# Optimization experiments

Hardware: AMD Instinct MI355X
Metric: run time of the kernel (lower is better)

## Reference

```python
import jax, jax.numpy as jnp
import numpy as np

B, T, E, H = 4, 1024, 768, 12
HD = E // H                      # 64
R = 2                            # lora rank
LORA_SCALE = 1.0 / R             # loralib default lora_alpha=1 -> alpha/r
NUM_BUCKETS, MAX_DIST = 320, 800


def _rel_bucket(rel):
    nb = NUM_BUCKETS // 2                      # 160
    buckets = (rel > 0).astype(jnp.int32) * nb
    rel = jnp.abs(rel)
    max_exact = nb // 2                        # 80
    is_small = rel < max_exact
    log_ratio = jnp.log(jnp.maximum(rel, 1).astype(jnp.float32) / max_exact)
    large = max_exact + (log_ratio / np.log(MAX_DIST / max_exact) * (nb - max_exact)).astype(jnp.int32)
    large = jnp.minimum(large, nb - 1)
    return buckets + jnp.where(is_small, rel, large)


def setup_inputs() -> dict:
    key = jax.random.key(0)
    ks = jax.random.split(key, 22)
    s = 0.02
    w = lambda k, shape: jax.random.normal(k, shape, jnp.float32) * s
    return {
        "hidden_states": jax.random.normal(ks[0], (B, T, E), jnp.float32),
        "Wq": w(ks[1], (E, E)), "bq": w(ks[2], (E,)),
        "Wk": w(ks[3], (E, E)), "bk": w(ks[4], (E,)),
        "Wv": w(ks[5], (E, E)), "bv": w(ks[6], (E,)),
        "Aq": w(ks[7], (R, E)), "Bq": w(ks[8], (E, R)),
        "Ak": w(ks[9], (R, E)), "Bk": w(ks[10], (E, R)),
        "Av": w(ks[11], (R, E)), "Bv": w(ks[12], (E, R)),
        "Wo": w(ks[13], (E, E)), "bo": w(ks[14], (E,)),
        "Wg": w(ks[15], (8, HD)), "bg": w(ks[16], (8,)),
        "gru_const": jnp.ones((1, H, 1, 1), jnp.float32),
        "rel_embed": w(ks[17], (NUM_BUCKETS, H)),
    }


def reference(hidden_states, Wq, bq, Wk, bk, Wv, bv,
              Aq, Bq, Ak, Bk, Av, Bv, Wo, bo, Wg, bg, gru_const, rel_embed):
    Bsz, Tq, _ = hidden_states.shape
    # --- relative position bias [H, T, T] ---
    pos = jnp.arange(Tq)
    bucket = _rel_bucket(pos[None, :] - pos[:, None])
    pos_bias = rel_embed[bucket].transpose(2, 0, 1)
    # --- dynamic gate from hidden states, per head/position ---
    g = hidden_states.reshape(Bsz, Tq, H, HD).transpose(0, 2, 1, 3)      # [B,H,T,hd]
    gp = jnp.einsum('bhtd,ed->bhte', g, Wg) + bg                          # [B,H,T,8]
    gp = gp.reshape(Bsz, H, Tq, 2, 4).sum(-1)                             # [B,H,T,2]
    gates = jax.nn.sigmoid(gp)
    gate_a, gate_b = gates[..., :1], gates[..., 1:]
    gate = gate_a * (gate_b * gru_const - 1.0) + 2.0                      # [B,H,T,1]
    gated_bias = gate * pos_bias[None]                                    # [B,H,T,T]
    # --- projections: original double-applies q/k/v_proj (proj+LoRA, then
    #     again inside F.multi_head_attention_forward via separate proj weights) ---
    lin = lambda x, W, b: jnp.einsum('bte,oe->bto', x, W) + b
    lora = lambda x, A, Bm: jnp.einsum('bte,re,or->bto', x, A, Bm) * LORA_SCALE
    x = hidden_states
    q1 = lin(x, Wq, bq) + lora(x, Aq, Bq)
    k1 = lin(x, Wk, bk) + lora(x, Ak, Bk)
    v1 = lin(x, Wv, bv) + lora(x, Av, Bv)
    q = lin(q1, Wq, bq) * (HD ** -0.5)
    k = lin(k1, Wk, bk)
    v = lin(v1, Wv, bv)
    qh = q.reshape(Bsz, Tq, H, HD).transpose(0, 2, 1, 3)
    kh = k.reshape(Bsz, Tq, H, HD).transpose(0, 2, 1, 3)
    vh = v.reshape(Bsz, Tq, H, HD).transpose(0, 2, 1, 3)
    scores = jnp.einsum('bhqd,bhkd->bhqk', qh, kh) + gated_bias
    attn = jax.nn.softmax(scores, axis=-1)
    ctx = jnp.einsum('bhqk,bhkd->bhqd', attn, vh)
    out = ctx.transpose(0, 2, 1, 3).reshape(Bsz, Tq, E)
    return jnp.einsum('bte,oe->bto', out, Wo) + bo
```

## Files before the change

### kernel.cpp

```cpp
#include <hip/hip_runtime.h>
#include <math.h>

#define TT 1024
#define EE 768
#define HH 12

typedef __attribute__((ext_vector_type(8))) __bf16 bf16x8;
typedef __attribute__((ext_vector_type(4))) float f32x4;

__device__ __forceinline__ unsigned short f2b(float f) {
    unsigned int u = __float_as_uint(f);
    unsigned int r = (u + 0x7fffu + ((u >> 16) & 1u)) >> 16;
    return (unsigned short)r;
}

#define GLD16(gsrc, ldst) \
    __builtin_amdgcn_global_load_lds( \
        (const __attribute__((address_space(1))) unsigned int*)(gsrc), \
        (__attribute__((address_space(3))) unsigned int*)(ldst), 16, 0, 0)

__global__ __launch_bounds__(256)
void setup_k(const float* __restrict__ hs,
             const float* __restrict__ Wq, const float* __restrict__ Wk,
             const float* __restrict__ Wv, const float* __restrict__ Wo,
             const float* __restrict__ bq, const float* __restrict__ bk,
             const float* __restrict__ bv,
             const float* __restrict__ Aq, const float* __restrict__ Ak,
             const float* __restrict__ Av,
             const float* __restrict__ Bq, const float* __restrict__ Bk,
             const float* __restrict__ Bv,
             const float* __restrict__ Wg, const float* __restrict__ bg,
             const float* __restrict__ gru, const float* __restrict__ rel,
             unsigned short* __restrict__ Wall_b, unsigned short* __restrict__ WT_all,
             float* __restrict__ biasTab, float* __restrict__ bias2,
             float* __restrict__ B2,
             unsigned short* __restrict__ hsb, float* __restrict__ gate,
             float* __restrict__ xA) {
    __shared__ __align__(16) char smem[78080];
    const int bid = blockIdx.x, tid = threadIdx.x;

    if (bid < 1152) {
        size_t base = (size_t)bid * 2048 + tid * 8;
        int mat = (int)(base / 589824);
        size_t local = base % 589824;
        const float* S = mat == 0 ? Wq : (mat == 1 ? Wk : (mat == 2 ? Wv : Wo));
        float4 a = *(const float4*)&S[local];
        float4 c = *(const float4*)&S[local + 4];
        unsigned short hb[8] __attribute__((aligned(16)));
        hb[0] = f2b(a.x); hb[1] = f2b(a.y); hb[2] = f2b(a.z); hb[3] = f2b(a.w);
        hb[4] = f2b(c.x); hb[5] = f2b(c.y); hb[6] = f2b(c.z); hb[7] = f2b(c.w);
        *(uint4*)&Wall_b[base] = *(const uint4*)hb;
    } else if (bid < 1260) {
        unsigned short* Ts = (unsigned short*)smem;
        int v = bid - 1152;
        int mat = v / 36, tile = v % 36;
        int tr = tile / 6, tc = tile % 6;
        const float* S = mat == 0 ? Wq : (mat == 1 ? Wk : Wv);
        #pragma unroll
        for (int i = 0; i < 16; ++i) {
            int idx = i * 256 + tid;
            int row = idx >> 5, col4 = (idx & 31) * 4;
            float4 f = *(const float4*)&S[(size_t)(tr * 128 + row) * EE + tc * 128 + col4];
            Ts[(col4 + 0) * 136 + row] = f2b(f.x);
            Ts[(col4 + 1) * 136 + row] = f2b(f.y);
            Ts[(col4 + 2) * 136 + row] = f2b(f.z);
            Ts[(col4 + 3) * 136 + row] = f2b(f.w);
        }
        __syncthreads();
        unsigned short* dst = WT_all + (size_t)mat * 589824;
        #pragma unroll
        for (int i = 0; i < 8; ++i) {
            int idx = i * 256 + tid;
            int rr = idx >> 4, cg = (idx & 15) * 8;
            *(uint4*)&dst[(size_t)(tc * 128 + rr) * EE + tr * 128 + cg] =
                *(const uint4*)&Ts[rr * 136 + cg];
        }
    } else if (bid < 1356) {
        int idx = (bid - 1260) * 256 + tid;
        if (idx < 2047 * 12) {
            int h = idx % 12;
            int rr = idx / 12;
            int relv = rr - 1023;
            int base = relv > 0 ? 160 : 0;
            int ar = relv < 0 ? -relv : relv;
            int bkt;
            if (ar < 80) bkt = base + ar;
            else {
                double lr = log((double)ar / 80.0);
                int large = 80 + (int)(lr / log(10.0) * 80.0);
                if (large > 159) large = 159;
                bkt = base + large;
            }
            biasTab[h * 2048 + rr] = rel[bkt * 12 + h];
        }
    } else if (bid < 1368) {
        float* bvS = (float*)smem;
        float* BmS = bvS + 768;
        int v = bid - 1356;
        int sel = v / 4, nb = (v % 4) * 192;
        const float* W = sel == 0 ? Wq : (sel == 1 ? Wk : Wv);
        const float* bvec = sel == 0 ? bq : (sel == 1 ? bk : bv);
        const float* Bm = sel == 0 ? Bq : (sel == 1 ? Bk : Bv);
        for (int i = tid; i < 768; i += 256) bvS[i] = bvec[i];
        for (int i = tid; i < 1536; i += 256) BmS[i] = Bm[i];
        __syncthreads();
        if (tid < 192) {
            int n = nb + tid;
            const float* Wrow = W + (size_t)n * EE;
            float a0 = 0.f, a1 = 0.f, a2 = 0.f;
            for (int o = 0; o < EE; o += 4) {
                float4 w = *(const float4*)&Wrow[o];
                a0 += w.x * bvS[o] + w.y * bvS[o + 1] + w.z * bvS[o + 2] + w.w * bvS[o + 3];
                a1 += w.x * BmS[o * 2] + w.y * BmS[o * 2 + 2] + w.z * BmS[o * 2 + 4] + w.w * BmS[o * 2 + 6];
                a2 += w.x * BmS[o * 2 + 1] + w.y * BmS[o * 2 + 3] + w.z * BmS[o * 2 + 5] + w.w * BmS[o * 2 + 7];
            }
            float sc = (sel == 0) ? 0.125f : 1.0f;
            bias2[sel * 768 + n] = (a0 + bvS[n]) * sc;
            B2[sel * 1536 + n * 2 + 0] = a1 * sc;
            B2[sel * 1536 + n * 2 + 1] = a2 * sc;
        }
    } else {
        float* rowF = (float*)smem;
        float* AS   = rowF + 16 * 772;
        float* WgS  = AS + 6 * 768;
        float* gpS  = WgS + 8 * 68;
        float* redS = gpS + 16 * 100;
        float* bgS  = redS + 4 * 96;
        float* gcS  = bgS + 8;
        const int m0 = (bid - 1368) * 16;

        for (int i = tid; i < 512; i += 256) WgS[(i >> 6) * 68 + (i & 63)] = Wg[i];
        for (int i = tid; i < 1152; i += 256) {
            int which = i / 192, c4 = (i % 192) * 4;
            const float* src = (which < 2 ? Aq : (which < 4 ? Ak : Av)) + (which & 1) * 768 + c4;
            float4 f = *(const float4*)src;
            AS[which * 768 + c4 + 0] = f.x; AS[which * 768 + c4 + 1] = f.y;
            AS[which * 768 + c4 + 2] = f.z; AS[which * 768 + c4 + 3] = f.w;
        }
        if (tid < 8)  bgS[tid] = bg[tid];
        if (tid < 12) gcS[tid] = gru[tid];
        #pragma unroll
        for (int i = 0; i < 12; ++i) {
            int idx = i * 256 + tid;
            int row = idx / 192, c4 = (idx % 192) * 4;
            float4 f = *(const float4*)&hs[(size_t)(m0 + row) * EE + c4];
            rowF[row * 772 + c4 + 0] = f.x; rowF[row * 772 + c4 + 1] = f.y;
            rowF[row * 772 + c4 + 2] = f.z; rowF[row * 772 + c4 + 3] = f.w;
            unsigned int lo = (unsigned int)f2b(f.x) | ((unsigned int)f2b(f.y) << 16);
            unsigned int hi = (unsigned int)f2b(f.z) | ((unsigned int)f2b(f.w) << 16);
            uint2 p; p.x = lo; p.y = hi;
            *(uint2*)&hsb[(size_t)(m0 + row) * EE + c4] = p;
        }
        __syncthreads();
        #pragma unroll
        for (int j = 0; j < 6; ++j) {
            int idx = j * 256 + tid;
            int row = idx & 15, q = idx >> 4;
            int h = q % 12, e = q / 12;
            const float* rp = &rowF[row * 772 + h * 64];
            const float* wp = &WgS[e * 68];
            float a = 0.f;
            #pragma unroll 16
            for (int d = 0; d < 64; ++d) a += rp[d] * wp[d];
            gpS[row * 100 + h * 8 + e] = a;
        }
        {
            int row = tid & 15, seg = tid >> 4;
            float s[6] = {0.f, 0.f, 0.f, 0.f, 0.f, 0.f};
            #pragma unroll 8
            for (int j = 0; j < 48; ++j) {
                int e = seg * 48 + j;
                float xv = rowF[row * 772 + e];
                s[0] += xv * AS[e];            s[1] += xv * AS[768 + e];
                s[2] += xv * AS[1536 + e];     s[3] += xv * AS[2304 + e];
                s[4] += xv * AS[3072 + e];     s[5] += xv * AS[3840 + e];
            }
            #pragma unroll
            for (int i = 0; i < 6; ++i) {
                s[i] += __shfl_xor(s[i], 16, 64);
                s[i] += __shfl_xor(s[i], 32, 64);
            }
            int lane = tid & 63, w = tid >> 6;
            if ((lane >> 4) == 0)
                #pragma unroll
                for (int i = 0; i < 6; ++i) redS[w * 96 + row * 6 + i] = s[i];
        }
        __syncthreads();
        if (tid < 96) {
            int row = tid / 6, i = tid % 6;
            float v = redS[row * 6 + i] + redS[96 + row * 6 + i] +
                      redS[192 + row * 6 + i] + redS[288 + row * 6 + i];
            int sel = i >> 1, r = i & 1;
            xA[sel * 8192 + (size_t)(m0 + row) * 2 + r] = v;
        }
        if (tid < 192) {
            int row = tid / 12, h = tid % 12;
            const float* gp = &gpS[row * 100 + h * 8];
            float s0 = gp[0] + gp[1] + gp[2] + gp[3] + bgS[0] + bgS[1] + bgS[2] + bgS[3];
            float s1 = gp[4] + gp[5] + gp[6] + gp[7] + bgS[4] + bgS[5] + bgS[6] + bgS[7];
            float ga = 1.f / (1.f + __expf(-s0));
            float gb = 1.f / (1.f + __expf(-s1));
            int m = m0 + row;
            int b = m >> 10, tp = m & 1023;
            gate[((size_t)b * HH + h) * TT + tp] = ga * (gb * gcS[h] - 1.0f) + 2.0f;
        }
    }
}

__global__ __launch_bounds__(256, 3)
void wgemm_k(const unsigned short* __restrict__ Wall_b,
             const unsigned short* __restrict__ WT_all,
             unsigned short* __restrict__ W2_all) {
    __shared__ unsigned short At[128 * 32];
    __shared__ unsigned short Bt[128 * 32];
    const int tid = threadIdx.x;
    const int bxx = blockIdx.x;
    const int sel = bxx / 36, tile = bxx % 36;
    const int row0 = (tile / 6) * 128, col0 = (tile % 6) * 128;
    const unsigned short* A = Wall_b + (size_t)sel * 589824;
    const unsigned short* Bw = WT_all + (size_t)sel * 589824;

    const int lane = tid & 63, wv = tid >> 6;
    const int wm = (wv & 1) * 64, wn = (wv >> 1) * 64;
    const int l15 = lane & 15, g8 = (lane >> 4) * 8;
    const int lr = lane >> 2, lc = (lane & 3) * 8;
    const int c0 = wv * 2, c1 = wv * 2 + 1;
    const unsigned short* Abase0 = A + (size_t)(row0 + c0 * 16 + lr) * EE + lc;
    const unsigned short* Abase1 = A + (size_t)(row0 + c1 * 16 + lr) * EE + lc;
    const unsigned short* Bbase0 = Bw + (size_t)(col0 + c0 * 16 + lr) * EE + lc;
    const unsigned short* Bbase1 = Bw + (size_t)(col0 + c1 * 16 + lr) * EE + lc;

    f32x4 zero4 = {0.f, 0.f, 0.f, 0.f};
    f32x4 acc[4][4];
    #pragma unroll
    for (int i = 0; i < 4; ++i)
        #pragma unroll
        for (int j = 0; j < 4; ++j) acc[i][j] = zero4;

    for (int kt = 0; kt < 768; kt += 32) {
        GLD16(Abase0 + kt, &At[c0 * 512]);
        GLD16(Abase1 + kt, &At[c1 * 512]);
        GLD16(Bbase0 + kt, &Bt[c0 * 512]);
        GLD16(Bbase1 + kt, &Bt[c1 * 512]);
        __syncthreads();
        bf16x8 af[4], bf[4];
        #pragma unroll
        for (int mt = 0; mt < 4; ++mt) af[mt] = *(const bf16x8*)&At[(wm + mt * 16 + l15) * 32 + g8];
        #pragma unroll
        for (int nt = 0; nt < 4; ++nt) bf[nt] = *(const bf16x8*)&Bt[(wn + nt * 16 + l15) * 32 + g8];
        #pragma unroll
        for (int mt = 0; mt < 4; ++mt)
            #pragma unroll
            for (int nt = 0; nt < 4; ++nt)
                acc[mt][nt] = __builtin_amdgcn_mfma_f32_16x16x32_bf16(af[mt], bf[nt], acc[mt][nt], 0, 0, 0);
        __syncthreads();
    }
    unsigned short* out = W2_all + (size_t)sel * 589824;
    const float sc = (sel == 0) ? 0.125f : 1.0f;
    const int g4 = (lane >> 4) * 4;
    #pragma unroll
    for (int mt = 0; mt < 4; ++mt)
        #pragma unroll
        for (int r = 0; r < 4; ++r) {
            int grow = row0 + wm + mt * 16 + g4 + r;
            #pragma unroll
            for (int nt = 0; nt < 4; ++nt) {
                int ncol = col0 + wn + nt * 16 + l15;
                out[(size_t)grow * EE + ncol] = f2b(acc[mt][nt][r] * sc);
            }
        }
}

__global__ __launch_bounds__(256, 3)
void qkv_gemm_k(const unsigned short* __restrict__ Aall,
                const unsigned short* __restrict__ W2_all,
                const float* __restrict__ bias2,
                const float* __restrict__ xA, const float* __restrict__ B2,
                unsigned short* __restrict__ qb, unsigned short* __restrict__ kb,
                unsigned short* __restrict__ vb) {
    __shared__ unsigned short At[128 * 32];
    __shared__ unsigned short Bt[128 * 32];
    const int tid = threadIdx.x;
    const int bx = blockIdx.x, by = blockIdx.y;
    const int sel = bx / 6;
    const int col0 = (bx % 6) * 128, row0 = by * 128;
    const unsigned short* Wb = W2_all + (size_t)sel * 589824;
    const float* bias = bias2 + sel * 768;

    const int lane = tid & 63, wv = tid >> 6;
    const int wm = (wv & 1) * 64, wn = (wv >> 1) * 64;
    const int l15 = lane & 15, g8 = (lane >> 4) * 8;
    const int lr = lane >> 2, lc = (lane & 3) * 8;
    const int c0 = wv * 2, c1 = wv * 2 + 1;
    const unsigned short* Abase0 = Aall + (size_t)(row0 + c0 * 16 + lr) * EE + lc;
    const unsigned short* Abase1 = Aall + (size_t)(row0 + c1 * 16 + lr) * EE + lc;
    const unsigned short* Bbase0 = Wb + (size_t)(col0 + c0 * 16 + lr) * EE + lc;
    const unsigned short* Bbase1 = Wb + (size_t)(col0 + c1 * 16 + lr) * EE + lc;

    f32x4 zero4 = {0.f, 0.f, 0.f, 0.f};
    f32x4 acc[4][4];
    #pragma unroll
    for (int i = 0; i < 4; ++i)
        #pragma unroll
        for (int j = 0; j < 4; ++j) acc[i][j] = zero4;

    for (int kt = 0; kt < 768; kt += 32) {
        GLD16(Abase0 + kt, &At[c0 * 512]);
        GLD16(Abase1 + kt, &At[c1 * 512]);
        GLD16(Bbase0 + kt, &Bt[c0 * 512]);
        GLD16(Bbase1 + kt, &Bt[c1 * 512]);
        __syncthreads();
        bf16x8 af[4], bf[4];
        #pragma unroll
        for (int mt = 0; mt < 4; ++mt) af[mt] = *(const bf16x8*)&At[(wm + mt * 16 + l15) * 32 + g8];
        #pragma unroll
        for (int nt = 0; nt < 4; ++nt) bf[nt] = *(const bf16x8*)&Bt[(wn + nt * 16 + l15) * 32 + g8];
        #pragma unroll
        for (int mt = 0; mt < 4; ++mt)
            #pragma unroll
            for (int nt = 0; nt < 4; ++nt)
                acc[mt][nt] = __builtin_amdgcn_mfma_f32_16x16x32_bf16(af[mt], bf[nt], acc[mt][nt], 0, 0, 0);
        __syncthreads();
    }

    unsigned short* dst = sel == 0 ? qb : (sel == 1 ? kb : vb);
    const float* Lbase = xA + sel * 8192;
    const float* B2s   = B2 + sel * 1536;
    const int g4 = (lane >> 4) * 4;
    #pragma unroll
    for (int mt = 0; mt < 4; ++mt) {
        #pragma unroll
        for (int r = 0; r < 4; ++r) {
            size_t grow = (size_t)row0 + wm + mt * 16 + g4 + r;
            float l0 = Lbase[grow * 2], l1 = Lbase[grow * 2 + 1];
            #pragma unroll
            for (int nt = 0; nt < 4; ++nt) {
                int ncol = col0 + wn + nt * 16 + l15;
                float c = acc[mt][nt][r] + bias[ncol]
                          + 0.5f * (l0 * B2s[ncol * 2] + l1 * B2s[ncol * 2 + 1]);
                dst[grow * EE + ncol] = f2b(c);
            }
        }
    }
}

__global__ __launch_bounds__(256)
void vT_k(const unsigned short* __restrict__ vb, unsigned short* __restrict__ Vtg) {
    __shared__ unsigned short Vs[64 * 72];
    const int tid = threadIdx.x;
    const int tt = blockIdx.x, h = blockIdx.y, b = blockIdx.z;
    const int r = tid >> 3, cc = (tid & 7) * 8;
    #pragma unroll
    for (int i = 0; i < 2; ++i) {
        int row = i * 32 + r;
        const unsigned short* vp = vb + (size_t)(b * TT + tt * 64 + row) * EE + h * 64 + cc;
        *(uint4*)&Vs[row * 72 + cc] = *(const uint4*)vp;
    }
    __syncthreads();
    #pragma unroll
    for (int i = 0; i < 2; ++i) {
        int d = i * 32 + r;
        unsigned short tmp[8] __attribute__((aligned(16)));
        #pragma unroll
        for (int j = 0; j < 8; ++j) tmp[j] = Vs[(cc + j) * 72 + d];
        *(uint4*)&Vtg[((size_t)(b * HH + h) * 64 + d) * TT + tt * 64 + cc] = *(const uint4*)tmp;
    }
}

__global__ __launch_bounds__(256, 4)
void attn_k(const unsigned short* __restrict__ qb, const unsigned short* __restrict__ kb,
            const unsigned short* __restrict__ Vtg, const float* __restrict__ gate,
            const float* __restrict__ biasTab, unsigned short* __restrict__ ctx) {
    __shared__ unsigned short Qs[64 * 72];
    __shared__ unsigned short Ks[64 * 72];
    __shared__ unsigned short Vt[64 * 72];
    __shared__ unsigned short Ps[64 * 72];
    const int tid = threadIdx.x;
    const int qt = blockIdx.x, h = blockIdx.y, b = blockIdx.z;

    const int srow = tid >> 2, scol = (tid & 3) * 16;
    {
        const unsigned short* qp = qb + ((size_t)(b * TT + qt * 64 + srow)) * EE + h * 64 + scol;
        *(uint4*)&Qs[srow * 72 + scol]     = *(const uint4*)qp;
        *(uint4*)&Qs[srow * 72 + scol + 8] = *(const uint4*)(qp + 8);
    }
    const int lane = tid & 63, wv = tid >> 6;
    const int m0 = wv * 16;
    const int l15 = lane & 15, g = lane >> 4;

    float li[4];
    f32x4 zero4 = {0.f, 0.f, 0.f, 0.f};
    f32x4 oa[4];
    #pragma unroll
    for (int r = 0; r < 4; ++r) li[r] = 0.f;
    #pragma unroll
    for (int nt = 0; nt < 4; ++nt) oa[nt] = zero4;
    float gv[4];
    #pragma unroll
    for (int r = 0; r < 4; ++r)
        gv[r] = gate[((size_t)(b * HH + h)) * TT + qt * 64 + m0 + 4 * g + r];

    const unsigned short* kpbase = kb + ((size_t)(b * TT + srow)) * EE + h * 64 + scol;
    const unsigned short* vpbase = Vtg + ((size_t)(b * HH + h) * 64 + srow) * TT + scol;
    const float* btab = biasTab + h * 2048 + 1023 + l15 - qt * 64 - m0 - 4 * g;

    uint4 kr0 = *(const uint4*)kpbase;
    uint4 kr1 = *(const uint4*)(kpbase + 8);
    uint4 vr0 = *(const uint4*)vpbase;
    uint4 vr1 = *(const uint4*)(vpbase + 8);

    for (int kt = 0; kt < 16; ++kt) {
        __syncthreads();
        *(uint4*)&Ks[srow * 72 + scol]     = kr0;
        *(uint4*)&Ks[srow * 72 + scol + 8] = kr1;
        *(uint4*)&Vt[srow * 72 + scol]     = vr0;
        *(uint4*)&Vt[srow * 72 + scol + 8] = vr1;
        __syncthreads();
        if (kt < 15) {
            const unsigned short* kp = kpbase + (size_t)(kt + 1) * 64 * EE;
            kr0 = *(const uint4*)kp;
            kr1 = *(const uint4*)(kp + 8);
            const unsigned short* vp = vpbase + (kt + 1) * 64;
            vr0 = *(const uint4*)vp;
            vr1 = *(const uint4*)(vp + 8);
        }
        f32x4 sa[4];
        #pragma unroll
        for (int nt = 0; nt < 4; ++nt) sa[nt] = zero4;
        bf16x8 aq0 = *(const bf16x8*)&Qs[(m0 + l15) * 72 + g * 8];
        bf16x8 aq1 = *(const bf16x8*)&Qs[(m0 + l15) * 72 + 32 + g * 8];
        #pragma unroll
        for (int nt = 0; nt < 4; ++nt) {
            bf16x8 bk0 = *(const bf16x8*)&Ks[(nt * 16 + l15) * 72 + g * 8];
            bf16x8 bk1 = *(const bf16x8*)&Ks[(nt * 16 + l15) * 72 + 32 + g * 8];
            sa[nt] = __builtin_amdgcn_mfma_f32_16x16x32_bf16(aq0, bk0, sa[nt], 0, 0, 0);
            sa[nt] = __builtin_amdgcn_mfma_f32_16x16x32_bf16(aq1, bk1, sa[nt], 0, 0, 0);
        }
        #pragma unroll
        for (int nt = 0; nt < 4; ++nt) {
            const float* bt = btab + kt * 64 + nt * 16;
            #pragma unroll
            for (int r = 0; r < 4; ++r) {
                float e = __expf(fmaf(gv[r], bt[-r], sa[nt][r]));
                li[r] += e;
                Ps[(m0 + 4 * g + r) * 72 + nt * 16 + l15] = f2b(e);
            }
        }
        bf16x8 ap0 = *(const bf16x8*)&Ps[(m0 + l15) * 72 + g * 8];
        bf16x8 ap1 = *(const bf16x8*)&Ps[(m0 + l15) * 72 + 32 + g * 8];
        #pragma unroll
        for (int nt = 0; nt < 4; ++nt) {
            bf16x8 bv0 = *(const bf16x8*)&Vt[(nt * 16 + l15) * 72 + g * 8];
            bf16x8 bv1 = *(const bf16x8*)&Vt[(nt * 16 + l15) * 72 + 32 + g * 8];
            oa[nt] = __builtin_amdgcn_mfma_f32_16x16x32_bf16(ap0, bv0, oa[nt], 0, 0, 0);
            oa[nt] = __builtin_amdgcn_mfma_f32_16x16x32_bf16(ap1, bv1, oa[nt], 0, 0, 0);
        }
    }
    __syncthreads();
    #pragma unroll
    for (int r = 0; r < 4; ++r) {
        #pragma unroll
        for (int msk = 1; msk < 16; msk <<= 1)
            li[r] += __shfl_xor(li[r], msk, 16);
    }
    #pragma unroll
    for (int nt = 0; nt < 4; ++nt)
        #pragma unroll
        for (int r = 0; r < 4; ++r)
            Ks[(m0 + 4 * g + r) * 72 + nt * 16 + l15] = f2b(oa[nt][r] / li[r]);
    __syncthreads();
    {
        unsigned short* cp = ctx + ((size_t)(b * TT + qt * 64 + srow)) * EE + h * 64 + scol;
        *(uint4*)cp       = *(const uint4*)&Ks[srow * 72 + scol];
        *(uint4*)(cp + 8) = *(const uint4*)&Ks[srow * 72 + scol + 8];
    }
}

__global__ __launch_bounds__(256, 4)
void out_gemm_k(const unsigned short* __restrict__ Aall,
                const unsigned short* __restrict__ Wob,
                const float* __restrict__ bo, float* __restrict__ outf) {
    __shared__ unsigned short At[64 * 32];
    __shared__ unsigned short Bt[128 * 32];
    const int tid = threadIdx.x;
    const int col0 = blockIdx.x * 128, row0 = blockIdx.y * 64;

    const int lane = tid & 63, wv = tid >> 6;
    const int wm = (wv & 1) * 32, wn = (wv >> 1) * 64;
    const int l15 = lane & 15, g8 = (lane >> 4) * 8;
    const int lr = lane >> 2, lc = (lane & 3) * 8;
    const int c0 = wv * 2, c1 = wv * 2 + 1;
    const unsigned short* Abase  = Aall + (size_t)(row0 + wv * 16 + lr) * EE + lc;
    const unsigned short* Bbase0 = Wob + (size_t)(col0 + c0 * 16 + lr) * EE + lc;
    const unsigned short* Bbase1 = Wob + (size_t)(col0 + c1 * 16 + lr) * EE + lc;

    f32x4 zero4 = {0.f, 0.f, 0.f, 0.f};
    f32x4 acc[2][4];
    #pragma unroll
    for (int i = 0; i < 2; ++i)
        #pragma unroll
        for (int j = 0; j < 4; ++j) acc[i][j] = zero4;

    for (int kt = 0; kt < 768; kt += 32) {
        GLD16(Abase + kt, &At[wv * 512]);
        GLD16(Bbase0 + kt, &Bt[c0 * 512]);
        GLD16(Bbase1 + kt, &Bt[c1 * 512]);
        __syncthreads();
        bf16x8 af[2], bf[4];
        #pragma unroll
        for (int mt = 0; mt < 2; ++mt) af[mt] = *(const bf16x8*)&At[(wm + mt * 16 + l15) * 32 + g8];
        #pragma unroll
        for (int nt = 0; nt < 4; ++nt) bf[nt] = *(const bf16x8*)&Bt[(wn + nt * 16 + l15) * 32 + g8];
        #pragma unroll
        for (int mt = 0; mt < 2; ++mt)
            #pragma unroll
            for (int nt = 0; nt < 4; ++nt)
                acc[mt][nt] = __builtin_amdgcn_mfma_f32_16x16x32_bf16(af[mt], bf[nt], acc[mt][nt], 0, 0, 0);
        __syncthreads();
    }
    const int g4 = (lane >> 4) * 4;
    #pragma unroll
    for (int mt = 0; mt < 2; ++mt)
        #pragma unroll
        for (int r = 0; r < 4; ++r) {
            size_t grow = (size_t)row0 + wm + mt * 16 + g4 + r;
            #pragma unroll
            for (int nt = 0; nt < 4; ++nt) {
                int ncol = col0 + wn + nt * 16 + l15;
                outf[grow * EE + ncol] = acc[mt][nt][r] + bo[ncol];
            }
        }
}

extern "C" void kernel_launch(void* const* d_in, const int* in_sizes, int n_in,
                              void* d_out, int out_size, void* d_ws, size_t ws_size,
                              hipStream_t stream) {
    const float* hs  = (const float*)d_in[0];
    const float* Wq  = (const float*)d_in[1];
    const float* bq  = (const float*)d_in[2];
    const float* Wk  = (const float*)d_in[3];
    const float* bk  = (const float*)d_in[4];
    const float* Wv  = (const float*)d_in[5];
    const float* bv  = (const float*)d_in[6];
    const float* Aq  = (const float*)d_in[7];
    const float* Bq  = (const float*)d_in[8];
    const float* Ak  = (const float*)d_in[9];
    const float* Bk  = (const float*)d_in[10];
    const float* Av  = (const float*)d_in[11];
    const float* Bv  = (const float*)d_in[12];
    const float* Wo  = (const float*)d_in[13];
    const float* bo  = (const float*)d_in[14];
    const float* Wg  = (const float*)d_in[15];
    const float* bg  = (const float*)d_in[16];
    const float* gru = (const float*)d_in[17];
    const float* rel = (const float*)d_in[18];

    float* ws = (float*)d_ws;
    float* gate    = ws;
    float* biasTab = gate + 49152;
    float* xA      = biasTab + 24576;
    float* bias2   = xA + 24576;
    float* B2      = bias2 + 2304;
    unsigned short* hsb    = (unsigned short*)(B2 + 4608);
    unsigned short* Wall_b = hsb + 3145728;
    unsigned short* WT_all = Wall_b + 4 * 589824;
    unsigned short* W2_all = WT_all + 3 * 589824;
    unsigned short* qb     = W2_all + 3 * 589824;
    unsigned short* kb     = qb + 3145728;
    unsigned short* vb     = kb + 3145728;
    unsigned short* Vtg    = vb + 3145728;
    unsigned short* ctxb   = Vtg + 3145728;

    setup_k<<<1624, 256, 0, stream>>>(hs, Wq, Wk, Wv, Wo, bq, bk, bv,
                                      Aq, Ak, Av, Bq, Bk, Bv, Wg, bg, gru, rel,
                                      Wall_b, WT_all, biasTab, bias2, B2,
                                      hsb, gate, xA);
    wgemm_k<<<108, 256, 0, stream>>>(Wall_b, WT_all, W2_all);
    qkv_gemm_k<<<dim3(18, 32), 256, 0, stream>>>(hsb, W2_all, bias2, xA, B2, qb, kb, vb);
    vT_k<<<dim3(16, 12, 4), 256, 0, stream>>>(vb, Vtg);
    attn_k<<<dim3(16, 12, 4), 256, 0, stream>>>(qb, kb, Vtg, gate, biasTab, ctxb);
    out_gemm_k<<<dim3(6, 64), 256, 0, stream>>>(ctxb, Wall_b + 3 * 589824, bo, (float*)d_out);
}
```

Measured before the change: 230.7 us.

## Split setup kernel and halve GEMM row tiles to fill more CUs

The monolithic setup kernel is split into three kernels: a flat fp32-to-bf16 converter for hidden states and weights, a transpose/bias/bucket-table kernel, and a gate/LoRA-down kernel working on 8-row blocks with less shared memory. The weight-product and QKV GEMMs drop their M tile from 128 to 64 rows, which doubles block counts and raises the occupancy hint to 4. The goal is more parallelism and better CU utilisation on small grids. In exchange it adds two kernel launches, reads hidden states twice, and loses some operand reuse per GEMM tile.

```diff
diff --git a/kernel.cpp b/kernel.cpp
--- a/kernel.cpp
+++ b/kernel.cpp
@@ -20,40 +20,38 @@
         (__attribute__((address_space(3))) unsigned int*)(ldst), 16, 0, 0)
 
 __global__ __launch_bounds__(256)
-void setup_k(const float* __restrict__ hs,
-             const float* __restrict__ Wq, const float* __restrict__ Wk,
-             const float* __restrict__ Wv, const float* __restrict__ Wo,
-             const float* __restrict__ bq, const float* __restrict__ bk,
-             const float* __restrict__ bv,
-             const float* __restrict__ Aq, const float* __restrict__ Ak,
-             const float* __restrict__ Av,
-             const float* __restrict__ Bq, const float* __restrict__ Bk,
-             const float* __restrict__ Bv,
-             const float* __restrict__ Wg, const float* __restrict__ bg,
-             const float* __restrict__ gru, const float* __restrict__ rel,
-             unsigned short* __restrict__ Wall_b, unsigned short* __restrict__ WT_all,
-             float* __restrict__ biasTab, float* __restrict__ bias2,
-             float* __restrict__ B2,
-             unsigned short* __restrict__ hsb, float* __restrict__ gate,
-             float* __restrict__ xA) {
-    __shared__ __align__(16) char smem[78080];
+void conv_k(const float* __restrict__ hs, const float* __restrict__ Wq,
+            const float* __restrict__ Wk, const float* __restrict__ Wv,
+            const float* __restrict__ Wo, unsigned short* __restrict__ out) {
+    size_t i = 4 * (size_t)(blockIdx.x * 256 + threadIdx.x);
+    if (i >= 5505024) return;
+    const float* src;
+    if (i < 3145728)      src = hs + i;
+    else if (i < 3735552) src = Wq + (i - 3145728);
+    else if (i < 4325376) src = Wk + (i - 3735552);
+    else if (i < 4915200) src = Wv + (i - 4325376);
+    else                  src = Wo + (i - 4915200);
+    float4 f = *(const float4*)src;
+    unsigned int lo = (unsigned int)f2b(f.x) | ((unsigned int)f2b(f.y) << 16);
+    unsigned int hi = (unsigned int)f2b(f.z) | ((unsigned int)f2b(f.w) << 16);
+    uint2 p; p.x = lo; p.y = hi;
+    *(uint2*)&out[i] = p;
+}
+
+__global__ __launch_bounds__(256)
+void wT2_k(const float* __restrict__ Wq, const float* __restrict__ Wk,
+           const float* __restrict__ Wv,
+           const float* __restrict__ bq, const float* __restrict__ bk,
+           const float* __restrict__ bv,
+           const float* __restrict__ Bq, const float* __restrict__ Bk,
+           const float* __restrict__ Bv, const float* __restrict__ rel,
+           unsigned short* __restrict__ WT_all, float* __restrict__ biasTab,
+           float* __restrict__ bias2, float* __restrict__ B2) {
+    __shared__ __align__(16) char smem[34816];
     const int bid = blockIdx.x, tid = threadIdx.x;
-
-    if (bid < 1152) {
-        size_t base = (size_t)bid * 2048 + tid * 8;
-        int mat = (int)(base / 589824);
-        size_t local = base % 589824;
-        const float* S = mat == 0 ? Wq : (mat == 1 ? Wk : (mat == 2 ? Wv : Wo));
-        float4 a = *(const float4*)&S[local];
-        float4 c = *(const float4*)&S[local + 4];
-        unsigned short hb[8] __attribute__((aligned(16)));
-        hb[0] = f2b(a.x); hb[1] = f2b(a.y); hb[2] = f2b(a.z); hb[3] = f2b(a.w);
-        hb[4] = f2b(c.x); hb[5] = f2b(c.y); hb[6] = f2b(c.z); hb[7] = f2b(c.w);
-        *(uint4*)&Wall_b[base] = *(const uint4*)hb;
-    } else if (bid < 1260) {
+    if (bid < 108) {
         unsigned short* Ts = (unsigned short*)smem;
-        int v = bid - 1152;
-        int mat = v / 36, tile = v % 36;
+        int mat = bid / 36, tile = bid % 36;
         int tr = tile / 6, tc = tile % 6;
         const float* S = mat == 0 ? Wq : (mat == 1 ? Wk : Wv);
         #pragma unroll
@@ -75,8 +73,8 @@
             *(uint4*)&dst[(size_t)(tc * 128 + rr) * EE + tr * 128 + cg] =
                 *(const uint4*)&Ts[rr * 136 + cg];
         }
-    } else if (bid < 1356) {
-        int idx = (bid - 1260) * 256 + tid;
+    } else if (bid < 204) {
+        int idx = (bid - 108) * 256 + tid;
         if (idx < 2047 * 12) {
             int h = idx % 12;
             int rr = idx / 12;
@@ -93,10 +91,10 @@
             }
             biasTab[h * 2048 + rr] = rel[bkt * 12 + h];
         }
-    } else if (bid < 1368) {
+    } else {
         float* bvS = (float*)smem;
         float* BmS = bvS + 768;
-        int v = bid - 1356;
+        int v = bid - 204;
         int sel = v / 4, nb = (v % 4) * 192;
         const float* W = sel == 0 ? Wq : (sel == 1 ? Wk : Wv);
         const float* bvec = sel == 0 ? bq : (sel == 1 ? bk : bv);
@@ -119,137 +117,139 @@
             B2[sel * 1536 + n * 2 + 0] = a1 * sc;
             B2[sel * 1536 + n * 2 + 1] = a2 * sc;
         }
-    } else {
-        float* rowF = (float*)smem;
-        float* AS   = rowF + 16 * 772;
-        float* WgS  = AS + 6 * 768;
-        float* gpS  = WgS + 8 * 68;
-        float* redS = gpS + 16 * 100;
-        float* bgS  = redS + 4 * 96;
-        float* gcS  = bgS + 8;
-        const int m0 = (bid - 1368) * 16;
-
-        for (int i = tid; i < 512; i += 256) WgS[(i >> 6) * 68 + (i & 63)] = Wg[i];
-        for (int i = tid; i < 1152; i += 256) {
-            int which = i / 192, c4 = (i % 192) * 4;
-            const float* src = (which < 2 ? Aq : (which < 4 ? Ak : Av)) + (which & 1) * 768 + c4;
-            float4 f = *(const float4*)src;
-            AS[which * 768 + c4 + 0] = f.x; AS[which * 768 + c4 + 1] = f.y;
-            AS[which * 768 + c4 + 2] = f.z; AS[which * 768 + c4 + 3] = f.w;
-        }
-        if (tid < 8)  bgS[tid] = bg[tid];
-        if (tid < 12) gcS[tid] = gru[tid];
-        #pragma unroll
-        for (int i = 0; i < 12; ++i) {
-            int idx = i * 256 + tid;
-            int row = idx / 192, c4 = (idx % 192) * 4;
-            float4 f = *(const float4*)&hs[(size_t)(m0 + row) * EE + c4];
-            rowF[row * 772 + c4 + 0] = f.x; rowF[row * 772 + c4 + 1] = f.y;
-            rowF[row * 772 + c4 + 2] = f.z; rowF[row * 772 + c4 + 3] = f.w;
-            unsigned int lo = (unsigned int)f2b(f.x) | ((unsigned int)f2b(f.y) << 16);
-            unsigned int hi = (unsigned int)f2b(f.z) | ((unsigned int)f2b(f.w) << 16);
-            uint2 p; p.x = lo; p.y = hi;
-            *(uint2*)&hsb[(size_t)(m0 + row) * EE + c4] = p;
-        }
-        __syncthreads();
-        #pragma unroll
-        for (int j = 0; j < 6; ++j) {
-            int idx = j * 256 + tid;
-            int row = idx & 15, q = idx >> 4;
-            int h = q % 12, e = q / 12;
-            const float* rp = &rowF[row * 772 + h * 64];
-            const float* wp = &WgS[e * 68];
-            float a = 0.f;
-            #pragma unroll 16
-            for (int d = 0; d < 64; ++d) a += rp[d] * wp[d];
-            gpS[row * 100 + h * 8 + e] = a;
-        }
-        {
-            int row = tid & 15, seg = tid >> 4;
-            float s[6] = {0.f, 0.f, 0.f, 0.f, 0.f, 0.f};
-            #pragma unroll 8
-            for (int j = 0; j < 48; ++j) {
-                int e = seg * 48 + j;
-                float xv = rowF[row * 772 + e];
-                s[0] += xv * AS[e];            s[1] += xv * AS[768 + e];
-                s[2] += xv * AS[1536 + e];     s[3] += xv * AS[2304 + e];
-                s[4] += xv * AS[3072 + e];     s[5] += xv * AS[3840 + e];
-            }
-            #pragma unroll
-            for (int i = 0; i < 6; ++i) {
-                s[i] += __shfl_xor(s[i], 16, 64);
-                s[i] += __shfl_xor(s[i], 32, 64);
-            }
-            int lane = tid & 63, w = tid >> 6;
-            if ((lane >> 4) == 0)
-                #pragma unroll
-                for (int i = 0; i < 6; ++i) redS[w * 96 + row * 6 + i] = s[i];
-        }
-        __syncthreads();
-        if (tid < 96) {
-            int row = tid / 6, i = tid % 6;
-            float v = redS[row * 6 + i] + redS[96 + row * 6 + i] +
-                      redS[192 + row * 6 + i] + redS[288 + row * 6 + i];
-            int sel = i >> 1, r = i & 1;
-            xA[sel * 8192 + (size_t)(m0 + row) * 2 + r] = v;
-        }
-        if (tid < 192) {
-            int row = tid / 12, h = tid % 12;
-            const float* gp = &gpS[row * 100 + h * 8];
-            float s0 = gp[0] + gp[1] + gp[2] + gp[3] + bgS[0] + bgS[1] + bgS[2] + bgS[3];
-            float s1 = gp[4] + gp[5] + gp[6] + gp[7] + bgS[4] + bgS[5] + bgS[6] + bgS[7];
-            float ga = 1.f / (1.f + __expf(-s0));
-            float gb = 1.f / (1.f + __expf(-s1));
-            int m = m0 + row;
-            int b = m >> 10, tp = m & 1023;
-            gate[((size_t)b * HH + h) * TT + tp] = ga * (gb * gcS[h] - 1.0f) + 2.0f;
-        }
-    }
-}
-
-__global__ __launch_bounds__(256, 3)
+    }
+}
+
+__global__ __launch_bounds__(256)
+void hs_k(const float* __restrict__ hs, const float* __restrict__ Wg,
+          const float* __restrict__ bg, const float* __restrict__ gru,
+          const float* __restrict__ Aq, const float* __restrict__ Ak,
+          const float* __restrict__ Av,
+          float* __restrict__ gate, float* __restrict__ xA) {
+    __shared__ float rowF[8 * 772];
+    __shared__ float AS[6 * 768];
+    __shared__ float WgS[8 * 68];
+    __shared__ float gpS[8 * 100];
+    __shared__ float redS[4 * 48];
+    __shared__ float bgS[8];
+    __shared__ float gcS[12];
+    const int tid = threadIdx.x;
+    const int m0 = blockIdx.x * 8;
+
+    for (int i = tid; i < 512; i += 256) WgS[(i >> 6) * 68 + (i & 63)] = Wg[i];
+    for (int i = tid; i < 1152; i += 256) {
+        int which = i / 192, c4 = (i % 192) * 4;
+        const float* src = (which < 2 ? Aq : (which < 4 ? Ak : Av)) + (which & 1) * 768 + c4;
+        float4 f = *(const float4*)src;
+        AS[which * 768 + c4 + 0] = f.x; AS[which * 768 + c4 + 1] = f.y;
+        AS[which * 768 + c4 + 2] = f.z; AS[which * 768 + c4 + 3] = f.w;
+    }
+    if (tid < 8)  bgS[tid] = bg[tid];
+    if (tid < 12) gcS[tid] = gru[tid];
+    #pragma unroll
+    for (int i = 0; i < 6; ++i) {
+        int idx = i * 256 + tid;
+        int row = idx / 192, c4 = (idx % 192) * 4;
+        float4 f = *(const float4*)&hs[(size_t)(m0 + row) * EE + c4];
+        rowF[row * 772 + c4 + 0] = f.x; rowF[row * 772 + c4 + 1] = f.y;
+        rowF[row * 772 + c4 + 2] = f.z; rowF[row * 772 + c4 + 3] = f.w;
+    }
+    __syncthreads();
+    #pragma unroll
+    for (int j = 0; j < 3; ++j) {
+        int idx = j * 256 + tid;
+        int row = idx & 7, q = idx >> 3;
+        int h = q % 12, e = q / 12;
+        const float* rp = &rowF[row * 772 + h * 64];
+        const float* wp = &WgS[e * 68];
+        float a = 0.f;
+        #pragma unroll 16
+        for (int d = 0; d < 64; ++d) a += rp[d] * wp[d];
+        gpS[row * 100 + h * 8 + e] = a;
+    }
+    {
+        int row = tid & 7, seg = tid >> 3;
+        float s[6] = {0.f, 0.f, 0.f, 0.f, 0.f, 0.f};
+        #pragma unroll 8
+        for (int j = 0; j < 24; ++j) {
+            int e = seg * 24 + j;
+            float xv = rowF[row * 772 + e];
+            s[0] += xv * AS[e];            s[1] += xv * AS[768 + e];
+            s[2] += xv * AS[1536 + e];     s[3] += xv * AS[2304 + e];
+            s[4] += xv * AS[3072 + e];     s[5] += xv * AS[3840 + e];
+        }
+        #pragma unroll
+        for (int i = 0; i < 6; ++i) {
+            s[i] += __shfl_xor(s[i], 8, 64);
+            s[i] += __shfl_xor(s[i], 16, 64);
+            s[i] += __shfl_xor(s[i], 32, 64);
+        }
+        int lane = tid & 63, w = tid >> 6;
+        if ((lane >> 3) == 0)
+            #pragma unroll
+            for (int i = 0; i < 6; ++i) redS[w * 48 + row * 6 + i] = s[i];
+    }
+    __syncthreads();
+    if (tid < 48) {
+        int row = tid / 6, i = tid % 6;
+        float v = redS[row * 6 + i] + redS[48 + row * 6 + i] +
+                  redS[96 + row * 6 + i] + redS[144 + row * 6 + i];
+        int sel = i >> 1, r = i & 1;
+        xA[sel * 8192 + (size_t)(m0 + row) * 2 + r] = v;
+    }
+    if (tid < 96) {
+        int row = tid / 12, h = tid % 12;
+        const float* gp = &gpS[row * 100 + h * 8];
+        float s0 = gp[0] + gp[1] + gp[2] + gp[3] + bgS[0] + bgS[1] + bgS[2] + bgS[3];
+        float s1 = gp[4] + gp[5] + gp[6] + gp[7] + bgS[4] + bgS[5] + bgS[6] + bgS[7];
+        float ga = 1.f / (1.f + __expf(-s0));
+        float gb = 1.f / (1.f + __expf(-s1));
+        int m = m0 + row;
+        int b = m >> 10, tp = m & 1023;
+        gate[((size_t)b * HH + h) * TT + tp] = ga * (gb * gcS[h] - 1.0f) + 2.0f;
+    }
+}
+
+__global__ __launch_bounds__(256, 4)
 void wgemm_k(const unsigned short* __restrict__ Wall_b,
              const unsigned short* __restrict__ WT_all,
              unsigned short* __restrict__ W2_all) {
-    __shared__ unsigned short At[128 * 32];
+    __shared__ unsigned short At[64 * 32];
     __shared__ unsigned short Bt[128 * 32];
     const int tid = threadIdx.x;
-    const int bxx = blockIdx.x;
-    const int sel = bxx / 36, tile = bxx % 36;
-    const int row0 = (tile / 6) * 128, col0 = (tile % 6) * 128;
+    const int sel = blockIdx.x / 72, tile = blockIdx.x % 72;
+    const int row0 = (tile / 6) * 64, col0 = (tile % 6) * 128;
     const unsigned short* A = Wall_b + (size_t)sel * 589824;
     const unsigned short* Bw = WT_all + (size_t)sel * 589824;
 
     const int lane = tid & 63, wv = tid >> 6;
-    const int wm = (wv & 1) * 64, wn = (wv >> 1) * 64;
+    const int wm = (wv & 1) * 32, wn = (wv >> 1) * 64;
     const int l15 = lane & 15, g8 = (lane >> 4) * 8;
     const int lr = lane >> 2, lc = (lane & 3) * 8;
     const int c0 = wv * 2, c1 = wv * 2 + 1;
-    const unsigned short* Abase0 = A + (size_t)(row0 + c0 * 16 + lr) * EE + lc;
-    const unsigned short* Abase1 = A + (size_t)(row0 + c1 * 16 + lr) * EE + lc;
+    const unsigned short* Abase  = A + (size_t)(row0 + wv * 16 + lr) * EE + lc;
     const unsigned short* Bbase0 = Bw + (size_t)(col0 + c0 * 16 + lr) * EE + lc;
     const unsigned short* Bbase1 = Bw + (size_t)(col0 + c1 * 16 + lr) * EE + lc;
 
     f32x4 zero4 = {0.f, 0.f, 0.f, 0.f};
-    f32x4 acc[4][4];
-    #pragma unroll
-    for (int i = 0; i < 4; ++i)
+    f32x4 acc[2][4];
+    #pragma unroll
+    for (int i = 0; i < 2; ++i)
         #pragma unroll
         for (int j = 0; j < 4; ++j) acc[i][j] = zero4;
 
     for (int kt = 0; kt < 768; kt += 32) {
-        GLD16(Abase0 + kt, &At[c0 * 512]);
-        GLD16(Abase1 + kt, &At[c1 * 512]);
+        GLD16(Abase + kt, &At[wv * 512]);
         GLD16(Bbase0 + kt, &Bt[c0 * 512]);
         GLD16(Bbase1 + kt, &Bt[c1 * 512]);
         __syncthreads();
-        bf16x8 af[4], bf[4];
-        #pragma unroll
-        for (int mt = 0; mt < 4; ++mt) af[mt] = *(const bf16x8*)&At[(wm + mt * 16 + l15) * 32 + g8];
+        bf16x8 af[2], bf[4];
+        #pragma unroll
+        for (int mt = 0; mt < 2; ++mt) af[mt] = *(const bf16x8*)&At[(wm + mt * 16 + l15) * 32 + g8];
         #pragma unroll
         for (int nt = 0; nt < 4; ++nt) bf[nt] = *(const bf16x8*)&Bt[(wn + nt * 16 + l15) * 32 + g8];
         #pragma unroll
-        for (int mt = 0; mt < 4; ++mt)
+        for (int mt = 0; mt < 2; ++mt)
             #pragma unroll
             for (int nt = 0; nt < 4; ++nt)
                 acc[mt][nt] = __builtin_amdgcn_mfma_f32_16x16x32_bf16(af[mt], bf[nt], acc[mt][nt], 0, 0, 0);
@@ -259,7 +259,7 @@
     const float sc = (sel == 0) ? 0.125f : 1.0f;
     const int g4 = (lane >> 4) * 4;
     #pragma unroll
-    for (int mt = 0; mt < 4; ++mt)
+    for (int mt = 0; mt < 2; ++mt)
         #pragma unroll
         for (int r = 0; r < 4; ++r) {
             int grow = row0 + wm + mt * 16 + g4 + r;
@@ -271,52 +271,50 @@
         }
 }
 
-__global__ __launch_bounds__(256, 3)
+__global__ __launch_bounds__(256, 4)
 void qkv_gemm_k(const unsigned short* __restrict__ Aall,
                 const unsigned short* __restrict__ W2_all,
                 const float* __restrict__ bias2,
                 const float* __restrict__ xA, const float* __restrict__ B2,
                 unsigned short* __restrict__ qb, unsigned short* __restrict__ kb,
                 unsigned short* __restrict__ vb) {
-    __shared__ unsigned short At[128 * 32];
+    __shared__ unsigned short At[64 * 32];
     __shared__ unsigned short Bt[128 * 32];
     const int tid = threadIdx.x;
     const int bx = blockIdx.x, by = blockIdx.y;
     const int sel = bx / 6;
-    const int col0 = (bx % 6) * 128, row0 = by * 128;
+    const int col0 = (bx % 6) * 128, row0 = by * 64;
     const unsigned short* Wb = W2_all + (size_t)sel * 589824;
     const float* bias = bias2 + sel * 768;
 
     const int lane = tid & 63, wv = tid >> 6;
-    const int wm = (wv & 1) * 64, wn = (wv >> 1) * 64;
+    const int wm = (wv & 1) * 32, wn = (wv >> 1) * 64;
     const int l15 = lane & 15, g8 = (lane >> 4) * 8;
     const int lr = lane >> 2, lc = (lane & 3) * 8;
     const int c0 = wv * 2, c1 = wv * 2 + 1;
-    const unsigned short* Abase0 = Aall + (size_t)(row0 + c0 * 16 + lr) * EE + lc;
-    const unsigned short* Abase1 = Aall + (size_t)(row0 + c1 * 16 + lr) * EE + lc;
+    const unsigned short* Abase  = Aall + (size_t)(row0 + wv * 16 + lr) * EE + lc;
     const unsigned short* Bbase0 = Wb + (size_t)(col0 + c0 * 16 + lr) * EE + lc;
     const unsigned short* Bbase1 = Wb + (size_t)(col0 + c1 * 16 + lr) * EE + lc;
 
     f32x4 zero4 = {0.f, 0.f, 0.f, 0.f};
-    f32x4 acc[4][4];
-    #pragma unroll
-    for (int i = 0; i < 4; ++i)
+    f32x4 acc[2][4];
+    #pragma unroll
+    for (int i = 0; i < 2; ++i)
         #pragma unroll
         for (int j = 0; j < 4; ++j) acc[i][j] = zero4;
 
     for (int kt = 0; kt < 768; kt += 32) {
-        GLD16(Abase0 + kt, &At[c0 * 512]);
-        GLD16(Abase1 + kt, &At[c1 * 512]);
+        GLD16(Abase + kt, &At[wv * 512]);
         GLD16(Bbase0 + kt, &Bt[c0 * 512]);
         GLD16(Bbase1 + kt, &Bt[c1 * 512]);
         __syncthreads();
-        bf16x8 af[4], bf[4];
-        #pragma unroll
-        for (int mt = 0; mt < 4; ++mt) af[mt] = *(const bf16x8*)&At[(wm + mt * 16 + l15) * 32 + g8];
+        bf16x8 af[2], bf[4];
+        #pragma unroll
+        for (int mt = 0; mt < 2; ++mt) af[mt] = *(const bf16x8*)&At[(wm + mt * 16 + l15) * 32 + g8];
         #pragma unroll
         for (int nt = 0; nt < 4; ++nt) bf[nt] = *(const bf16x8*)&Bt[(wn + nt * 16 + l15) * 32 + g8];
         #pragma unroll
-        for (int mt = 0; mt < 4; ++mt)
+        for (int mt = 0; mt < 2; ++mt)
             #pragma unroll
             for (int nt = 0; nt < 4; ++nt)
                 acc[mt][nt] = __builtin_amdgcn_mfma_f32_16x16x32_bf16(af[mt], bf[nt], acc[mt][nt], 0, 0, 0);
@@ -328,7 +326,7 @@
     const float* B2s   = B2 + sel * 1536;
     const int g4 = (lane >> 4) * 4;
     #pragma unroll
-    for (int mt = 0; mt < 4; ++mt) {
+    for (int mt = 0; mt < 2; ++mt) {
         #pragma unroll
         for (int r = 0; r < 4; ++r) {
             size_t grow = (size_t)row0 + wm + mt * 16 + g4 + r;
@@ -571,12 +569,12 @@
     unsigned short* Vtg    = vb + 3145728;
     unsigned short* ctxb   = Vtg + 3145728;
 
-    setup_k<<<1624, 256, 0, stream>>>(hs, Wq, Wk, Wv, Wo, bq, bk, bv,
-                                      Aq, Ak, Av, Bq, Bk, Bv, Wg, bg, gru, rel,
-                                      Wall_b, WT_all, biasTab, bias2, B2,
-                                      hsb, gate, xA);
-    wgemm_k<<<108, 256, 0, stream>>>(Wall_b, WT_all, W2_all);
-    qkv_gemm_k<<<dim3(18, 32), 256, 0, stream>>>(hsb, W2_all, bias2, xA, B2, qb, kb, vb);
+    conv_k<<<5376, 256, 0, stream>>>(hs, Wq, Wk, Wv, Wo, hsb);
+    wT2_k<<<216, 256, 0, stream>>>(Wq, Wk, Wv, bq, bk, bv, Bq, Bk, Bv, rel,
+                                   WT_all, biasTab, bias2, B2);
+    hs_k<<<512, 256, 0, stream>>>(hs, Wg, bg, gru, Aq, Ak, Av, gate, xA);
+    wgemm_k<<<216, 256, 0, stream>>>(Wall_b, WT_all, W2_all);
+    qkv_gemm_k<<<dim3(18, 64), 256, 0, stream>>>(hsb, W2_all, bias2, xA, B2, qb, kb, vb);
     vT_k<<<dim3(16, 12, 4), 256, 0, stream>>>(vb, Vtg);
     attn_k<<<dim3(16, 12, 4), 256, 0, stream>>>(qb, kb, Vtg, gate, biasTab, ctxb);
     out_gemm_k<<<dim3(6, 64), 256, 0, stream>>>(ctxb, Wall_b + 3 * 589824, bo, (float*)d_out);
```

After: 241.8 us. 1.05x slower.
